# Kernel tuning notes

Measured on AMD Instinct MI355X. Metric: run time of the kernel, lower is better.

Reference implementation:

```python
import jax, jax.numpy as jnp
import numpy as np

B, C, E, S, L, N = 2, 256, 256, 3, 5, 128
HMAX = 128
LEVEL_SIZES = np.array([128, 64, 32, 16, 8])
STRIDES = np.array([8.0, 16.0, 32.0, 64.0, 128.0])
GROUPS = 8
EPS = 1e-5


def setup_inputs() -> dict:
    key = jax.random.key(0)
    ks = jax.random.split(key, 16)
    # Padded FPN pyramid stacked as [L, B, C, HMAX, HMAX]; level l valid in [:sz, :sz]
    fm = jnp.zeros((L, B, C, HMAX, HMAX), jnp.float32)
    for l in range(L):
        sz = int(LEVEL_SIZES[l])
        fm = fm.at[l, :, :, :sz, :sz].set(jax.random.normal(ks[l], (B, C, sz, sz), jnp.float32))
    # Boxes in 1024x1024 image coordinates (x1, y1, x2, y2)
    cxy = jax.random.uniform(ks[5], (N, 2), minval=60.0, maxval=960.0)
    wh = jax.random.uniform(ks[6], (N, 2), minval=8.0, maxval=96.0)
    boxes = jnp.concatenate([cxy - wh / 2, cxy + wh / 2], axis=1)
    batch_idx = jax.random.randint(ks[7], (N,), 0, B, jnp.int32)
    level_idx = jax.random.randint(ks[8], (N,), 0, L, jnp.int32)
    sym_ids = jax.random.randint(ks[9], (N,), 0, 6, jnp.int32)
    conv_w = jax.random.normal(ks[10], (E, C, 3, 3), jnp.float32) / np.float32(np.sqrt(C * 9))
    gn_scale = jnp.ones((E,), jnp.float32)
    gn_bias = jnp.zeros((E,), jnp.float32)
    head_w = jax.random.normal(ks[11], (E, E), jnp.float32) / np.float32(np.sqrt(E))
    head_b = jnp.zeros((E,), jnp.float32)
    spat_w = jax.random.normal(ks[12], (E, 4), jnp.float32) * 0.01
    spat_b = jnp.zeros((E,), jnp.float32)
    sym_emb = jax.random.normal(ks[13], (6, E), jnp.float32) * 0.05
    fuse_w = jax.random.normal(ks[14], (6, E, E), jnp.float32) / np.float32(np.sqrt(E))
    fuse_b = jnp.zeros((6, E), jnp.float32)
    return dict(feature_maps=fm, boxes=boxes, conv_w=conv_w, gn_scale=gn_scale,
                gn_bias=gn_bias, head_w=head_w, head_b=head_b, spat_w=spat_w,
                spat_b=spat_b, sym_emb=sym_emb, fuse_w=fuse_w, fuse_b=fuse_b,
                batch_idx=batch_idx, level_idx=level_idx, sym_ids=sym_ids)


def _roi_align(fm, boxes, batch_idx, level_idx):
    # Batched roi_align (aligned=False, sampling_ratio=1) over all boxes at once.
    scale = (1.0 / jnp.asarray(STRIDES, fm.dtype))[level_idx]          # [N]
    hv = jnp.asarray(LEVEL_SIZES, fm.dtype)[level_idx]                 # [N] valid H=W per box
    x1 = boxes[:, 0] * scale; y1 = boxes[:, 1] * scale
    x2 = boxes[:, 2] * scale; y2 = boxes[:, 3] * scale
    roi_w = jnp.maximum(x2 - x1, 1.0)
    roi_h = jnp.maximum(y2 - y1, 1.0)
    off = (jnp.arange(S, dtype=fm.dtype) + 0.5) / S                    # bin centers
    xs = x1[:, None] + off[None, :] * roi_w[:, None]                   # [N,S]
    ys = y1[:, None] + off[None, :] * roi_h[:, None]                   # [N,S]
    y = jnp.broadcast_to(ys[:, :, None], (ys.shape[0], S, S))          # [N,S,S]
    x = jnp.broadcast_to(xs[:, None, :], (xs.shape[0], S, S))
    hvb = hv[:, None, None]
    valid = (y > -1.0) & (y < hvb) & (x > -1.0) & (x < hvb)
    yc = jnp.clip(y, 0.0, hvb - 1.0)
    xc = jnp.clip(x, 0.0, hvb - 1.0)
    y0 = jnp.floor(yc).astype(jnp.int32)
    x0 = jnp.floor(xc).astype(jnp.int32)
    hi = (hvb - 1.0).astype(jnp.int32)
    y1i = jnp.minimum(y0 + 1, hi)
    x1i = jnp.minimum(x0 + 1, hi)
    ly = yc - y0.astype(fm.dtype)
    lx = xc - x0.astype(fm.dtype)
    lvl = level_idx[:, None, None]
    bix = batch_idx[:, None, None]

    def g(yi, xi):
        # gather only the 4 corner pixels -> [N,S,S,C]
        return fm[lvl, bix, :, yi, xi]

    v = ((1 - ly) * (1 - lx))[..., None] * g(y0, x0) \
      + ((1 - ly) * lx)[..., None] * g(y0, x1i) \
      + (ly * (1 - lx))[..., None] * g(y1i, x0) \
      + (ly * lx)[..., None] * g(y1i, x1i)
    v = jnp.where(valid[..., None], v, 0.0)
    return jnp.transpose(v, (0, 3, 1, 2))                              # [N,C,S,S]


def _forward(feature_maps, boxes, conv_w, gn_scale, gn_bias, head_w, head_b,
             spat_w, spat_b, sym_emb, fuse_w, fuse_b, batch_idx, level_idx, sym_ids):
    roi = _roi_align(feature_maps, boxes, batch_idx, level_idx)        # [N,C,S,S]
    h = jax.lax.conv_general_dilated(roi, conv_w, (1, 1), ((1, 1), (1, 1)),
                                     dimension_numbers=('NCHW', 'OIHW', 'NCHW'))  # [N,E,S,S]
    n = h.shape[0]
    hg = h.reshape(n, GROUPS, -1)
    mu = hg.mean(-1, keepdims=True)
    var = hg.var(-1, keepdims=True)
    hg = (hg - mu) * jax.lax.rsqrt(var + EPS)
    h = hg.reshape(h.shape) * gn_scale[None, :, None, None] + gn_bias[None, :, None, None]
    h = jax.nn.relu(h)
    h = h.reshape(n, E, -1).mean(-1)                                   # spatial mean -> [N,E]
    head_out = jax.nn.relu(h @ head_w.T + head_b)                      # sym_feat_nn + ReLU
    spat = jax.nn.relu(boxes @ spat_w.T + spat_b)                      # spatial_embeddings
    fused_in = head_out + spat + sym_emb[sym_ids]                      # + class embedding
    out = jax.nn.relu(jnp.einsum('ne,nfe->nf', fused_in, fuse_w[sym_ids]) + fuse_b[sym_ids])
    return out                                                          # [N,E]


def reference(feature_maps, boxes, conv_w, gn_scale, gn_bias, head_w, head_b,
              spat_w, spat_b, sym_emb, fuse_w, fuse_b, batch_idx, level_idx, sym_ids):
    return _forward(feature_maps, boxes, conv_w, gn_scale, gn_bias, head_w, head_b,
                    spat_w, spat_b, sym_emb, fuse_w, fuse_b, batch_idx, level_idx, sym_ids)
```

## Files before the change

### kernel.cpp

```cpp
#include <hip/hip_runtime.h>
#include <hip/hip_bf16.h>


typedef float v2f __attribute__((ext_vector_type(2)));

__device__ __forceinline__ float bf_lo(unsigned u) { return __uint_as_float(u << 16); }
__device__ __forceinline__ float bf_hi(unsigned u) { return __uint_as_float(u & 0xffff0000u); }
__device__ __forceinline__ unsigned short f2bf(float f) {
    __hip_bfloat16 h = __float2bfloat16(f);
    return *(unsigned short*)&h;
}

__global__ __launch_bounds__(256) void prep_k(
    const float* __restrict__ conv_w,
    const float* __restrict__ head_w, const float* __restrict__ fuse_w,
    const float* __restrict__ fm, const float* __restrict__ boxes,
    const int* __restrict__ batch_idx, const int* __restrict__ level_idx,
    unsigned short* __restrict__ w8, unsigned short* __restrict__ w9,
    unsigned short* __restrict__ head_wTb, unsigned short* __restrict__ fuse_wTb,
    float* __restrict__ roiT) {
    int blk = blockIdx.x;
    int t = threadIdx.x;

    if (blk < 256) {
        int c = blk, e = t;
        const float* src = conv_w + ((size_t)e * 256 + c) * 9;
        unsigned short tmp[8];
#pragma unroll
        for (int k = 0; k < 8; ++k) tmp[k] = f2bf(src[k]);
        ((uint4*)w8)[(size_t)c * 256 + e] = *(const uint4*)tmp;
        w9[(size_t)c * 256 + e] = f2bf(src[8]);
        return;
    }

    if (blk < 704) {
        __shared__ float tile[32][33];
        int q = blk - 256;
        int z = q >> 6;
        int rem = q & 63;
        int bx = (rem & 7) * 32, by = (rem >> 3) * 32;
        const float* in = (z == 0) ? head_w : fuse_w + (size_t)(z - 1) * 65536;
        unsigned short* out = (z == 0) ? head_wTb : fuse_wTb + (size_t)(z - 1) * 65536;
        int tx = t & 31, ty = t >> 5;
#pragma unroll
        for (int i = 0; i < 32; i += 8)
            tile[ty + i][tx] = in[(size_t)(by + ty + i) * 256 + bx + tx];
        __syncthreads();
#pragma unroll
        for (int i = 0; i < 32; i += 8) {
            int k = bx + ty + i;
            int e = by + tx;
            out[(size_t)((k >> 1) * 256 + e) * 2 + (k & 1)] = f2bf(tile[tx][ty + i]);
        }
        return;
    }

    {
        int q = blk - 704;
        int n = q & 127, p = q >> 7;
        int i = p / 3, j = p % 3;
        int c = t;

        int lvl = level_idx[n];
        int b = batch_idx[n];
        const float sizes[5]  = {128.f, 64.f, 32.f, 16.f, 8.f};
        const float invstr[5] = {1.f/8.f, 1.f/16.f, 1.f/32.f, 1.f/64.f, 1.f/128.f};
        float scale = invstr[lvl];
        float hv = sizes[lvl];

        float x1 = boxes[n*4+0] * scale, y1 = boxes[n*4+1] * scale;
        float x2 = boxes[n*4+2] * scale, y2 = boxes[n*4+3] * scale;
        float rw = fmaxf(x2 - x1, 1.f), rh = fmaxf(y2 - y1, 1.f);
        float x = x1 + (((float)j + 0.5f) / 3.f) * rw;
        float y = y1 + (((float)i + 0.5f) / 3.f) * rh;

        bool valid = (y > -1.f) && (y < hv) && (x > -1.f) && (x < hv);
        float yc = fminf(fmaxf(y, 0.f), hv - 1.f);
        float xc = fminf(fmaxf(x, 0.f), hv - 1.f);
        int y0 = (int)floorf(yc), x0 = (int)floorf(xc);
        int hi = (int)(hv - 1.f);
        int y1i = min(y0 + 1, hi), x1i = min(x0 + 1, hi);
        float ly = yc - (float)y0, lx = xc - (float)x0;

        const float* base = fm + (((size_t)lvl * 2 + b) * 256 + c) * (128 * 128);
        float v00 = base[y0 * 128 + x0];
        float v01 = base[y0 * 128 + x1i];
        float v10 = base[y1i * 128 + x0];
        float v11 = base[y1i * 128 + x1i];
        float v = (1.f - ly) * (1.f - lx) * v00 + (1.f - ly) * lx * v01 +
                  ly * (1.f - lx) * v10 + ly * lx * v11;
        roiT[((size_t)n * 9 + p) * 256 + c] = valid ? v : 0.f;
    }
}

__global__ __launch_bounds__(512, 2) void conv_gn_head(
    const float* __restrict__ roiT,
    const unsigned short* __restrict__ w8, const unsigned short* __restrict__ w9,
    const float* __restrict__ gn_scale, const float* __restrict__ gn_bias,
    const float* __restrict__ boxes,
    const unsigned short* __restrict__ head_wTb, const float* __restrict__ head_b,
    const float* __restrict__ spat_w, const float* __restrict__ spat_b,
    const float* __restrict__ sym_emb,
    const unsigned short* __restrict__ fuse_wTb, const float* __restrict__ fuse_b,
    const int* __restrict__ sym_ids, float* __restrict__ out) {
    __shared__ v2f red[2 * 128 * 9];
    __shared__ float pl[256];
    __shared__ float part[512];
    __shared__ float fin[256];

    int n = blockIdx.x;
    int t = threadIdx.x;
    int ep = t & 127;
    int ch = __builtin_amdgcn_readfirstlane(t >> 7);

    const float* r = roiT + (size_t)n * 2304;

    v2f acc[9];
#pragma unroll
    for (int p = 0; p < 9; ++p) acc[p] = (v2f)(0.f);

    int c0 = ch * 64;
#pragma unroll 2
    for (int c = c0; c < c0 + 64; c += 2) {
        v2f q[9];
#pragma unroll
        for (int jj = 0; jj < 9; ++jj)
            q[jj] = *(const v2f*)(r + jj * 256 + c);

#pragma unroll
        for (int cc = 0; cc < 2; ++cc) {
            int cw = c + cc;
            uint4 wa = ((const uint4*)w8)[(size_t)cw * 256 + ep];
            uint4 wb = ((const uint4*)w8)[(size_t)cw * 256 + ep + 128];
            v2f w2[9];
            w2[0].x = bf_lo(wa.x); w2[0].y = bf_lo(wb.x);
            w2[1].x = bf_hi(wa.x); w2[1].y = bf_hi(wb.x);
            w2[2].x = bf_lo(wa.y); w2[2].y = bf_lo(wb.y);
            w2[3].x = bf_hi(wa.y); w2[3].y = bf_hi(wb.y);
            w2[4].x = bf_lo(wa.z); w2[4].y = bf_lo(wb.z);
            w2[5].x = bf_hi(wa.z); w2[5].y = bf_hi(wb.z);
            w2[6].x = bf_lo(wa.w); w2[6].y = bf_lo(wb.w);
            w2[7].x = bf_hi(wa.w); w2[7].y = bf_hi(wb.w);
            w2[8].x = bf_lo((unsigned)w9[(size_t)cw * 256 + ep]);
            w2[8].y = bf_lo((unsigned)w9[(size_t)cw * 256 + ep + 128]);

            v2f rr[9];
#pragma unroll
            for (int jj = 0; jj < 9; ++jj) {
                float rv = cc ? q[jj].y : q[jj].x;
                rr[jj].x = rv; rr[jj].y = rv;
            }
#pragma unroll
            for (int ky = 0; ky < 3; ++ky) {
#pragma unroll
                for (int kx = 0; kx < 3; ++kx) {
                    v2f wk = w2[ky * 3 + kx];
#pragma unroll
                    for (int oy = 0; oy < 3; ++oy) {
                        int iy = oy + ky - 1;
                        if (iy < 0 || iy > 2) continue;
#pragma unroll
                        for (int ox = 0; ox < 3; ++ox) {
                            int ix = ox + kx - 1;
                            if (ix < 0 || ix > 2) continue;
                            int o = oy * 3 + ox, in = iy * 3 + ix;
                            acc[o] = wk * rr[in] + acc[o];
                        }
                    }
                }
            }
        }
    }

    if (ch >= 2) {
#pragma unroll
        for (int p = 0; p < 9; ++p)
            red[((ch - 2) * 128 + ep) * 9 + p] = acc[p];
    }
    __syncthreads();
    if (ch < 2) {
#pragma unroll
        for (int p = 0; p < 9; ++p)
            acc[p] += red[(ch * 128 + ep) * 9 + p];
    }
    __syncthreads();
    if (ch == 1) {
#pragma unroll
        for (int p = 0; p < 9; ++p)
            red[ep * 9 + p] = acc[p];
    }
    __syncthreads();

    if (ch == 0) {
#pragma unroll
        for (int p = 0; p < 9; ++p)
            acc[p] += red[ep * 9 + p];

        v2f s = (v2f)(0.f), sq = (v2f)(0.f);
#pragma unroll
        for (int p = 0; p < 9; ++p) { s += acc[p]; sq += acc[p] * acc[p]; }
#pragma unroll
        for (int m = 16; m >= 1; m >>= 1) {
            s.x  += __shfl_xor(s.x,  m, 64);
            s.y  += __shfl_xor(s.y,  m, 64);
            sq.x += __shfl_xor(sq.x, m, 64);
            sq.y += __shfl_xor(sq.y, m, 64);
        }
        float mean0 = s.x * (1.f / 288.f), mean1 = s.y * (1.f / 288.f);
        float var0 = sq.x * (1.f / 288.f) - mean0 * mean0;
        float var1 = sq.y * (1.f / 288.f) - mean1 * mean1;
        float ri0 = rsqrtf(var0 + 1e-5f), ri1 = rsqrtf(var1 + 1e-5f);
        float gs0 = gn_scale[ep],       gb0 = gn_bias[ep];
        float gs1 = gn_scale[ep + 128], gb1 = gn_bias[ep + 128];
        float ps0 = 0.f, ps1 = 0.f;
#pragma unroll
        for (int p = 0; p < 9; ++p) {
            float v0 = (acc[p].x - mean0) * ri0 * gs0 + gb0;
            float v1 = (acc[p].y - mean1) * ri1 * gs1 + gb1;
            ps0 += fmaxf(v0, 0.f);
            ps1 += fmaxf(v1, 0.f);
        }
        pl[ep]       = ps0 * (1.f / 9.f);
        pl[ep + 128] = ps1 * (1.f / 9.f);
    }
    __syncthreads();

    int e = t & 255;
    int kh = t >> 8;
    int sid = sym_ids[n];

    {
        float a2 = 0.f;
        const unsigned* w = (const unsigned*)head_wTb + (size_t)(kh * 64) * 256 + e;
        const float* p = pl + kh * 128;
#pragma unroll 8
        for (int kp = 0; kp < 64; ++kp) {
            unsigned u = w[kp * 256];
            a2 = fmaf(p[2 * kp],     bf_lo(u), a2);
            a2 = fmaf(p[2 * kp + 1], bf_hi(u), a2);
        }
        part[t] = a2;
    }
    __syncthreads();
    if (t < 256) {
        float ho = fmaxf(part[t] + part[t + 256] + head_b[t], 0.f);
        float4 sw = ((const float4*)spat_w)[t];
        float b0 = boxes[n*4+0], b1 = boxes[n*4+1], b2 = boxes[n*4+2], b3 = boxes[n*4+3];
        float sp = fmaxf(spat_b[t] + b0*sw.x + b1*sw.y + b2*sw.z + b3*sw.w, 0.f);
        fin[t] = ho + sp + sym_emb[sid * 256 + t];
    }
    __syncthreads();
    {
        float o = 0.f;
        const unsigned* w = (const unsigned*)fuse_wTb + (size_t)sid * 32768
                            + (size_t)(kh * 64) * 256 + e;
        const float* p = fin + kh * 128;
#pragma unroll 8
        for (int kp = 0; kp < 64; ++kp) {
            unsigned u = w[kp * 256];
            o = fmaf(p[2 * kp],     bf_lo(u), o);
            o = fmaf(p[2 * kp + 1], bf_hi(u), o);
        }
        part[t] = o;
    }
    __syncthreads();
    if (t < 256)
        out[(size_t)n * 256 + t] = fmaxf(part[t] + part[t + 256] + fuse_b[sid * 256 + t], 0.f);
}

extern "C" void kernel_launch(void* const* d_in, const int* in_sizes, int n_in,
                              void* d_out, int out_size, void* d_ws, size_t ws_size,
                              hipStream_t stream) {
    const float* fm      = (const float*)d_in[0];
    const float* boxes   = (const float*)d_in[1];
    const float* conv_w  = (const float*)d_in[2];
    const float* gn_s    = (const float*)d_in[3];
    const float* gn_b    = (const float*)d_in[4];
    const float* head_w  = (const float*)d_in[5];
    const float* head_b  = (const float*)d_in[6];
    const float* spat_w  = (const float*)d_in[7];
    const float* spat_b  = (const float*)d_in[8];
    const float* sym_emb = (const float*)d_in[9];
    const float* fuse_w  = (const float*)d_in[10];
    const float* fuse_b  = (const float*)d_in[11];
    const int* batch_idx = (const int*)d_in[12];
    const int* level_idx = (const int*)d_in[13];
    const int* sym_ids   = (const int*)d_in[14];
    float* outp = (float*)d_out;

    char* ws = (char*)d_ws;
    unsigned short* w8       = (unsigned short*)ws;
    unsigned short* w9       = (unsigned short*)(ws + 1048576);
    unsigned short* head_wTb = (unsigned short*)(ws + 1179648);
    unsigned short* fuse_wTb = (unsigned short*)(ws + 1310720);
    float* roiT    = (float*)(ws + 2097152);

    prep_k<<<1856, 256, 0, stream>>>(conv_w, head_w, fuse_w, fm, boxes,
                                     batch_idx, level_idx,
                                     w8, w9, head_wTb, fuse_wTb, roiT);
    conv_gn_head<<<128, 512, 0, stream>>>(roiT, w8, w9, gn_s, gn_b, boxes,
                                          head_wTb, head_b, spat_w, spat_b,
                                          sym_emb, fuse_wTb, fuse_b, sym_ids, outp);
}
```

Baseline: 257.3 us.

## Transpose feature pyramid to channel-last and fuse RoI sampling into conv kernel

The prep kernel now transposes every valid pyramid level into a channel-last buffer instead of computing RoI samples. The conv kernel then does the bilinear RoI sampling itself, with coalesced per-channel reads into LDS, and no longer stages a roiT buffer in global memory. This aims to make the gather reads coalesced and drop a global round trip. The cost is a full read and write of the whole pyramid on every call, which is much more memory traffic than the sparse gather it replaces.

```diff
diff --git a/kernel.cpp b/kernel.cpp
--- a/kernel.cpp
+++ b/kernel.cpp
@@ -11,14 +11,15 @@
     return *(unsigned short*)&h;
 }
 
+__constant__ int VOFF_c[5] = {0, 32768, 40960, 43008, 43520};
+
 __global__ __launch_bounds__(256) void prep_k(
     const float* __restrict__ conv_w,
     const float* __restrict__ head_w, const float* __restrict__ fuse_w,
-    const float* __restrict__ fm, const float* __restrict__ boxes,
-    const int* __restrict__ batch_idx, const int* __restrict__ level_idx,
+    const float* __restrict__ fm,
     unsigned short* __restrict__ w8, unsigned short* __restrict__ w9,
     unsigned short* __restrict__ head_wTb, unsigned short* __restrict__ fuse_wTb,
-    float* __restrict__ roiT) {
+    float* __restrict__ fmT) {
     int blk = blockIdx.x;
     int t = threadIdx.x;
 
@@ -56,64 +57,101 @@
     }
 
     {
-        int q = blk - 704;
-        int n = q & 127, p = q >> 7;
-        int i = p / 3, j = p % 3;
-        int c = t;
-
+        __shared__ float tile[64][129];
+        int r = blk - 704;
+        int l, base;
+        if      (r < 256) { l = 0; base = 0;   }
+        else if (r < 384) { l = 1; base = 256; }
+        else if (r < 448) { l = 2; base = 384; }
+        else if (r < 480) { l = 3; base = 448; }
+        else              { l = 4; base = 480; }
+        int szi = 128 >> l;
+        int local = r - base;
+        int b = (local >= szi) ? 1 : 0;
+        int y = local - b * szi;
+
+        size_t src_row = ((size_t)(l * 2 + b) * 256) * 16384 + (size_t)y * 128;
+        size_t dst_vec0 = (size_t)VOFF_c[l] + (size_t)b * szi * szi + (size_t)y * szi;
+
+        int lane = t & 63, cq = t >> 6;
+        for (int c0 = 0; c0 < 256; c0 += 64) {
+#pragma unroll
+            for (int i = 0; i < 16; ++i) {
+                int cl = cq * 16 + i;
+                size_t sa = src_row + (size_t)(c0 + cl) * 16384;
+                if (lane < szi) tile[cl][lane] = fm[sa + lane];
+                if (szi == 128) tile[cl][lane + 64] = fm[sa + lane + 64];
+            }
+            __syncthreads();
+            int cc = t & 63, xq = t >> 6;
+            for (int x = xq; x < szi; x += 4)
+                fmT[(dst_vec0 + x) * 256 + c0 + cc] = tile[cc][x];
+            __syncthreads();
+        }
+    }
+}
+
+__global__ __launch_bounds__(512, 2) void conv_gn_head(
+    const float* __restrict__ fmT, const float* __restrict__ boxes,
+    const int* __restrict__ batch_idx, const int* __restrict__ level_idx,
+    const unsigned short* __restrict__ w8, const unsigned short* __restrict__ w9,
+    const float* __restrict__ gn_scale, const float* __restrict__ gn_bias,
+    const unsigned short* __restrict__ head_wTb, const float* __restrict__ head_b,
+    const float* __restrict__ spat_w, const float* __restrict__ spat_b,
+    const float* __restrict__ sym_emb,
+    const unsigned short* __restrict__ fuse_wTb, const float* __restrict__ fuse_b,
+    const int* __restrict__ sym_ids, float* __restrict__ out) {
+    __shared__ float roi_lds[9 * 256];
+    __shared__ v2f red[2 * 128 * 9];
+    __shared__ float pl[256];
+    __shared__ float part[512];
+    __shared__ float fin[256];
+
+    int n = blockIdx.x;
+    int t = threadIdx.x;
+
+    {
+        int c = t & 255;
+        int ph = t >> 8;
         int lvl = level_idx[n];
         int b = batch_idx[n];
         const float sizes[5]  = {128.f, 64.f, 32.f, 16.f, 8.f};
         const float invstr[5] = {1.f/8.f, 1.f/16.f, 1.f/32.f, 1.f/64.f, 1.f/128.f};
         float scale = invstr[lvl];
         float hv = sizes[lvl];
-
-        float x1 = boxes[n*4+0] * scale, y1 = boxes[n*4+1] * scale;
-        float x2 = boxes[n*4+2] * scale, y2 = boxes[n*4+3] * scale;
-        float rw = fmaxf(x2 - x1, 1.f), rh = fmaxf(y2 - y1, 1.f);
-        float x = x1 + (((float)j + 0.5f) / 3.f) * rw;
-        float y = y1 + (((float)i + 0.5f) / 3.f) * rh;
-
-        bool valid = (y > -1.f) && (y < hv) && (x > -1.f) && (x < hv);
-        float yc = fminf(fmaxf(y, 0.f), hv - 1.f);
-        float xc = fminf(fmaxf(x, 0.f), hv - 1.f);
-        int y0 = (int)floorf(yc), x0 = (int)floorf(xc);
-        int hi = (int)(hv - 1.f);
-        int y1i = min(y0 + 1, hi), x1i = min(x0 + 1, hi);
-        float ly = yc - (float)y0, lx = xc - (float)x0;
-
-        const float* base = fm + (((size_t)lvl * 2 + b) * 256 + c) * (128 * 128);
-        float v00 = base[y0 * 128 + x0];
-        float v01 = base[y0 * 128 + x1i];
-        float v10 = base[y1i * 128 + x0];
-        float v11 = base[y1i * 128 + x1i];
-        float v = (1.f - ly) * (1.f - lx) * v00 + (1.f - ly) * lx * v01 +
-                  ly * (1.f - lx) * v10 + ly * lx * v11;
-        roiT[((size_t)n * 9 + p) * 256 + c] = valid ? v : 0.f;
-    }
-}
-
-__global__ __launch_bounds__(512, 2) void conv_gn_head(
-    const float* __restrict__ roiT,
-    const unsigned short* __restrict__ w8, const unsigned short* __restrict__ w9,
-    const float* __restrict__ gn_scale, const float* __restrict__ gn_bias,
-    const float* __restrict__ boxes,
-    const unsigned short* __restrict__ head_wTb, const float* __restrict__ head_b,
-    const float* __restrict__ spat_w, const float* __restrict__ spat_b,
-    const float* __restrict__ sym_emb,
-    const unsigned short* __restrict__ fuse_wTb, const float* __restrict__ fuse_b,
-    const int* __restrict__ sym_ids, float* __restrict__ out) {
-    __shared__ v2f red[2 * 128 * 9];
-    __shared__ float pl[256];
-    __shared__ float part[512];
-    __shared__ float fin[256];
-
-    int n = blockIdx.x;
-    int t = threadIdx.x;
+        int szi = 128 >> lvl;
+        size_t base_vec = (size_t)VOFF_c[lvl] + (size_t)b * szi * szi;
+
+        float bx1 = boxes[n*4+0] * scale, by1 = boxes[n*4+1] * scale;
+        float bx2 = boxes[n*4+2] * scale, by2 = boxes[n*4+3] * scale;
+        float rw = fmaxf(bx2 - bx1, 1.f), rh = fmaxf(by2 - by1, 1.f);
+
+        int pend = ph ? 9 : 5;
+        for (int p = ph * 5; p < pend; ++p) {
+            int i = p / 3, j = p % 3;
+            float x = bx1 + (((float)j + 0.5f) / 3.f) * rw;
+            float y = by1 + (((float)i + 0.5f) / 3.f) * rh;
+            bool valid = (y > -1.f) && (y < hv) && (x > -1.f) && (x < hv);
+            float yc = fminf(fmaxf(y, 0.f), hv - 1.f);
+            float xc = fminf(fmaxf(x, 0.f), hv - 1.f);
+            int y0 = (int)floorf(yc), x0 = (int)floorf(xc);
+            int hi = szi - 1;
+            int y1i = min(y0 + 1, hi), x1i = min(x0 + 1, hi);
+            float ly = yc - (float)y0, lx = xc - (float)x0;
+
+            float v00 = fmT[(base_vec + y0  * szi + x0 ) * 256 + c];
+            float v01 = fmT[(base_vec + y0  * szi + x1i) * 256 + c];
+            float v10 = fmT[(base_vec + y1i * szi + x0 ) * 256 + c];
+            float v11 = fmT[(base_vec + y1i * szi + x1i) * 256 + c];
+            float v = (1.f - ly) * (1.f - lx) * v00 + (1.f - ly) * lx * v01 +
+                      ly * (1.f - lx) * v10 + ly * lx * v11;
+            roi_lds[p * 256 + c] = valid ? v : 0.f;
+        }
+    }
+    __syncthreads();
+
     int ep = t & 127;
     int ch = __builtin_amdgcn_readfirstlane(t >> 7);
-
-    const float* r = roiT + (size_t)n * 2304;
 
     v2f acc[9];
 #pragma unroll
@@ -125,7 +163,7 @@
         v2f q[9];
 #pragma unroll
         for (int jj = 0; jj < 9; ++jj)
-            q[jj] = *(const v2f*)(r + jj * 256 + c);
+            q[jj] = *(const v2f*)(&roi_lds[jj * 256 + c]);
 
 #pragma unroll
         for (int cc = 0; cc < 2; ++cc) {
@@ -293,12 +331,12 @@
     unsigned short* w9       = (unsigned short*)(ws + 1048576);
     unsigned short* head_wTb = (unsigned short*)(ws + 1179648);
     unsigned short* fuse_wTb = (unsigned short*)(ws + 1310720);
-    float* roiT    = (float*)(ws + 2097152);
-
-    prep_k<<<1856, 256, 0, stream>>>(conv_w, head_w, fuse_w, fm, boxes,
-                                     batch_idx, level_idx,
-                                     w8, w9, head_wTb, fuse_wTb, roiT);
-    conv_gn_head<<<128, 512, 0, stream>>>(roiT, w8, w9, gn_s, gn_b, boxes,
+    float* fmT     = (float*)(ws + 2097152);
+
+    prep_k<<<1200, 256, 0, stream>>>(conv_w, head_w, fuse_w, fm,
+                                     w8, w9, head_wTb, fuse_wTb, fmT);
+    conv_gn_head<<<128, 512, 0, stream>>>(fmT, boxes, batch_idx, level_idx,
+                                          w8, w9, gn_s, gn_b,
                                           head_wTb, head_b, spat_w, spat_b,
                                           sym_emb, fuse_wTb, fuse_b, sym_ids, outp);
 }
```

Measured after the change: 333.2 us. +29.5%, slower.
